# Optimization experiments

Measured on AMD Instinct MI355X. Metric: run time of the kernel, lower is better.

The kernel has to match this reference:

```python
import jax, jax.numpy as jnp
import numpy as np

GRID = 64
N_NODES = GRID * GRID
LN_EPS = 1e-5


def _grid_edge_index(n=GRID):
    ids = np.arange(n * n, dtype=np.int32).reshape(n, n)
    r0, r1 = ids[:, :-1].ravel(), ids[:, 1:].ravel()   # horizontal neighbors
    d0, d1 = ids[:-1, :].ravel(), ids[1:, :].ravel()   # vertical neighbors
    src = np.concatenate([r0, r1, d0, d1])
    dst = np.concatenate([r1, r0, d1, d0])
    return np.stack([src, dst])  # [2, 16128] directed edges


def setup_inputs() -> dict:
    key = jax.random.key(0)
    ks = jax.random.split(key, 6)
    B, C, H, L = 128, 12, 64, 3
    s_in = 1.0 / np.sqrt(C)
    s_h = 1.0 / np.sqrt(H)
    return {
        "x": jax.random.normal(ks[0], (B, C, GRID, GRID), jnp.float32),
        "edge_index": jnp.asarray(_grid_edge_index()),
        "w_in": jax.random.normal(ks[1], (C, H), jnp.float32) * s_in,
        "b_in": jnp.zeros((H,), jnp.float32),
        "w_self": jax.random.normal(ks[2], (L, H, H), jnp.float32) * s_h,
        "w_neigh": jax.random.normal(ks[3], (L, H, H), jnp.float32) * s_h,
        "conv_b": jnp.zeros((L, H), jnp.float32),
        "ln_g": jnp.ones((L, H), jnp.float32),
        "ln_b": jnp.zeros((L, H), jnp.float32),
        "w_head": jax.random.normal(ks[4], (H, 1), jnp.float32) * s_h,
        "b_head": jnp.zeros((1,), jnp.float32),
    }


def reference(x, edge_index, w_in, b_in, w_self, w_neigh, conv_b, ln_g, ln_b, w_head, b_head):
    B = x.shape[0]
    BN = B * N_NODES
    # grid_to_nodes: [B, C, 64, 64] -> [B, N, C]
    nodes = jnp.transpose(x, (0, 2, 3, 1)).reshape(B, N_NODES, -1)
    h = (nodes @ w_in + b_in).reshape(BN, -1)
    # batched_edge_index: replicate with per-graph node offsets
    offs = (jnp.arange(B, dtype=edge_index.dtype) * N_NODES)
    ei = (edge_index[:, None, :] + offs[None, :, None]).reshape(2, -1)
    src, dst = ei[0], ei[1]
    deg = jax.ops.segment_sum(jnp.ones_like(src, dtype=h.dtype), dst, num_segments=BN)
    inv_deg = (1.0 / jnp.maximum(deg, 1.0))[:, None]
    n_layers = w_self.shape[0]
    for l in range(n_layers):
        # SAGE-mean conv: gather src feats, scatter-sum to dst, mean-normalize
        agg = jax.ops.segment_sum(h[src], dst, num_segments=BN) * inv_deg
        hn = h @ w_self[l] + agg @ w_neigh[l] + conv_b[l]
        mu = hn.mean(-1, keepdims=True)
        var = ((hn - mu) ** 2).mean(-1, keepdims=True)
        hn = (hn - mu) * jax.lax.rsqrt(var + LN_EPS) * ln_g[l] + ln_b[l]
        h = h + jax.nn.relu(hn)  # dropout is identity in eval mode
    logit = (h @ w_head + b_head).reshape(B, GRID, GRID)
    return logit
```

## Files before the change

### kernel.cpp

```cpp
#include <hip/hip_runtime.h>

#define GRID_D 64
#define NN (GRID_D * GRID_D)
#define H 64
#define C_IN 12
#define B_SZ 128
#define LN_EPS 1e-5f

typedef _Float16 f16x8 __attribute__((ext_vector_type(8)));
typedef _Float16 f16x4 __attribute__((ext_vector_type(4)));
typedef float    f32x4 __attribute__((ext_vector_type(4)));

#define AS1 __attribute__((address_space(1)))
#define AS3 __attribute__((address_space(3)))

__global__ __launch_bounds__(256) void k_prep(
    const float* __restrict__ ws_, const float* __restrict__ wn_,
    _Float16* __restrict__ wt)
{
    int i = blockIdx.x * 256 + threadIdx.x;
    if (i < 3 * 2 * 4096) {
        int l = i >> 13, g = (i >> 12) & 1, j = (i >> 6) & 63, k = i & 63;
        const float* W = (g ? wn_ : ws_) + l * 4096;
        wt[i] = (_Float16)W[k * 64 + j];
    }
}

__global__ __launch_bounds__(256) void k_inproj(
    const float* __restrict__ x, const float* __restrict__ w_in,
    const float* __restrict__ b_in, _Float16* __restrict__ h)
{
    int bid = blockIdx.x;
    int b = bid >> 6, r = bid & 63;
    __shared__ float xs[C_IN][GRID_D];
    __shared__ float ws[C_IN][H];
    int tid = threadIdx.x;
    const float* xb = x + (size_t)b * C_IN * NN + (size_t)r * GRID_D;
    for (int idx = tid; idx < C_IN * GRID_D; idx += 256) {
        int c = idx >> 6, n = idx & 63;
        xs[c][n] = xb[(size_t)c * NN + n];
        ws[c][n] = w_in[idx];
    }
    __syncthreads();
    int n = tid >> 2;
    int j0 = (tid & 3) * 16;
    float acc[16];
    #pragma unroll
    for (int t = 0; t < 16; ++t) acc[t] = b_in[j0 + t];
    #pragma unroll
    for (int c = 0; c < C_IN; ++c) {
        float xv = xs[c][n];
        #pragma unroll
        for (int t = 0; t < 16; ++t) acc[t] += xv * ws[c][j0 + t];
    }
    _Float16* hp = h + (size_t)(b * NN + r * GRID_D + n) * H + j0;
    f16x8 o0, o1;
    #pragma unroll
    for (int t = 0; t < 8; ++t) { o0[t] = (_Float16)acc[t]; o1[t] = (_Float16)acc[8 + t]; }
    *(f16x8*)hp = o0;
    *(f16x8*)(hp + 8) = o1;
}

__device__ __forceinline__ void stage_row(
    const _Float16* hb, int grow, _Float16* slot, int wv, int ln)
{
    const _Float16* src = hb
        + (((size_t)(grow * GRID_D + wv * 8 + (ln >> 3))) << 6)
        + (((ln & 7) ^ (ln >> 3)) << 3);
    _Float16* dst = slot + wv * 512;
    __builtin_amdgcn_global_load_lds((const AS1 void*)src, (AS3 void*)dst, 16, 0, 0);
}

__global__ __launch_bounds__(768, 3) void k_fused(
    const _Float16* __restrict__ h0, float* __restrict__ logits,
    const _Float16* __restrict__ wtb,
    const float* __restrict__ cb, const float* __restrict__ lg,
    const float* __restrict__ lb,
    const float* __restrict__ w_head, const float* __restrict__ b_head)
{
    __shared__ _Float16 ring[3][4][4096];
    __shared__ float    pl[640];

    int tid = threadIdx.x, ln = tid & 63, wv = tid >> 6;
    int bid = blockIdx.x;
    int img = bid >> 1, chunk = bid & 1;
    int r0 = chunk << 5;
    const _Float16* hb = h0 + ((size_t)img << 18);

    int grp = wv >> 2;
    int ct  = wv & 3;
    int lrow = ln & 15, kgrp = ln >> 4;
    int col = ct * 16 + lrow;
    int cs = col & 7;
    int kq = kgrp * 4;
    bool cl = (col > 0), cr = (col < 63);

    const _Float16* wg = wtb + grp * 8192;
    f16x8 wsf[2][4], wnf[2][4];
    #pragma unroll
    for (int ks = 0; ks < 2; ++ks) {
        int k0 = ks * 32 + kq * 2;
        #pragma unroll
        for (int ft = 0; ft < 4; ++ft) {
            int j = ft * 16 + lrow;
            wsf[ks][ft] = *(const f16x8*)(wg + (j << 6) + k0);
            wnf[ks][ft] = *(const f16x8*)(wg + ((64 + j) << 6) + k0);
        }
    }
    #pragma unroll
    for (int ks = 0; ks < 2; ++ks)
        #pragma unroll
        for (int ft = 0; ft < 4; ++ft)
            asm volatile("" : "+v"(wsf[ks][ft]), "+v"(wnf[ks][ft]));

    if (tid < 576) {
        int l = tid / 192, r = tid % 192;
        pl[tid] = (r < 64) ? cb[l * 64 + r]
                : (r < 128) ? lg[l * 64 + r - 64] : lb[l * 64 + r - 128];
    } else if (tid < 640) {
        pl[tid] = w_head[tid - 576];
    }

    const float* myp = pl + grp * 192;
    float bh = b_head[0];

    int lo0 = (r0 - 3 < 0) ? 0 : r0 - 3, hi0 = (r0 + 34 > 63) ? 63 : r0 + 34;
    int loC, hiC;
    if (grp == 0)      { loC = (r0 - 2 < 0) ? 0 : r0 - 2; hiC = (r0 + 33 > 63) ? 63 : r0 + 33; }
    else if (grp == 1) { loC = (r0 - 1 < 0) ? 0 : r0 - 1; hiC = (r0 + 32 > 63) ? 63 : r0 + 32; }
    else               { loC = r0;                         hiC = r0 + 31; }

    _Float16* rin  = &ring[grp][0][0];
    _Float16* rout = (grp < 2) ? &ring[grp + 1][0][0] : nullptr;

    #pragma unroll 1
    for (int s = 0; s <= 40; ++s) {
        int p0 = r0 - 3 + s;
        if (wv < 8 && p0 >= lo0 && p0 <= hi0)
            stage_row(hb, p0, &ring[0][p0 & 3][0], wv, ln);

        int pr = p0 - 2 * grp - 2;
        if (pr >= loC && pr <= hiC) {
            const _Float16* rc = rin + ((pr & 3) << 12);
            const _Float16* ru = rin + (((pr - 1) & 3) << 12);
            const _Float16* rd = rin + (((pr + 1) & 3) << 12);
            _Float16 hinv = (_Float16)(1.0f / (float)((pr > 0) + (pr < 63) + cl + cr));

            f32x4 acc[4];
            #pragma unroll
            for (int ft = 0; ft < 4; ++ft) acc[ft] = (f32x4){0.f, 0.f, 0.f, 0.f};

            #pragma unroll
            for (int ks = 0; ks < 2; ++ks) {
                int sl = ((ks * 4 + kgrp) ^ cs) << 3;
                f16x8 a = *(const f16x8*)(rc + (col << 6) + sl);
                #pragma unroll
                for (int ft = 0; ft < 4; ++ft)
                    acc[ft] = __builtin_amdgcn_mfma_f32_16x16x32_f16(wsf[ks][ft], a, acc[ft], 0, 0, 0);
            }

            #pragma unroll
            for (int ks = 0; ks < 2; ++ks) {
                int c8 = ks * 4 + kgrp;
                int sl = (c8 ^ cs) << 3;
                f16x8 z = {};
                f16x8 u = (pr > 0)  ? *(const f16x8*)(ru + (col << 6) + sl) : z;
                f16x8 d = (pr < 63) ? *(const f16x8*)(rd + (col << 6) + sl) : z;
                int cm = col - cl;
                f16x8 lv = *(const f16x8*)(rc + (cm << 6) + ((c8 ^ (cm & 7)) << 3));
                if (!cl) lv = z;
                int cp = col + cr;
                f16x8 rv = *(const f16x8*)(rc + (cp << 6) + ((c8 ^ (cp & 7)) << 3));
                if (!cr) rv = z;
                f16x8 sm = (lv + rv) + (u + d);
                f16x8 g;
                #pragma unroll
                for (int e = 0; e < 8; ++e) g[e] = sm[e] * hinv;
                #pragma unroll
                for (int ft = 0; ft < 4; ++ft)
                    acc[ft] = __builtin_amdgcn_mfma_f32_16x16x32_f16(wnf[ks][ft], g, acc[ft], 0, 0, 0);
            }

            float s1 = 0.f, s2 = 0.f;
            #pragma unroll
            for (int ft = 0; ft < 4; ++ft) {
                f32x4 q = *(const f32x4*)&myp[ft * 16 + kq];
                acc[ft] += q;
                #pragma unroll
                for (int t = 0; t < 4; ++t) { float xv = acc[ft][t]; s1 += xv; s2 += xv * xv; }
            }
            s1 += __shfl_xor(s1, 16); s1 += __shfl_xor(s1, 32);
            s2 += __shfl_xor(s2, 16); s2 += __shfl_xor(s2, 32);
            float mu   = s1 * (1.0f / H);
            float var  = s2 * (1.0f / H) - mu * mu;
            float rstd = rsqrtf(var + LN_EPS);

            const _Float16* res = rc + (col << 6);
            if (grp < 2) {
                _Float16* outp = rout + ((pr & 3) << 12) + (col << 6);
                #pragma unroll
                for (int ft = 0; ft < 4; ++ft) {
                    f32x4 lgq = *(const f32x4*)&myp[64 + ft * 16 + kq];
                    f32x4 lbq = *(const f32x4*)&myp[128 + ft * 16 + kq];
                    int slot = (ft * 2 + (kgrp >> 1)) ^ cs;
                    f16x4 rq = *(const f16x4*)(res + (slot << 3) + (kgrp & 1) * 4);
                    f16x4 oq;
                    #pragma unroll
                    for (int t = 0; t < 4; ++t) {
                        float o = (float)rq[t]
                                + fmaxf((acc[ft][t] - mu) * rstd * lgq[t] + lbq[t], 0.f);
                        oq[t] = (_Float16)o;
                    }
                    *(f16x4*)(outp + (slot << 3) + (kgrp & 1) * 4) = oq;
                }
            } else {
                float part = 0.f;
                #pragma unroll
                for (int ft = 0; ft < 4; ++ft) {
                    f32x4 lgq = *(const f32x4*)&myp[64 + ft * 16 + kq];
                    f32x4 lbq = *(const f32x4*)&myp[128 + ft * 16 + kq];
                    f32x4 whq = *(const f32x4*)&pl[576 + ft * 16 + kq];
                    int slot = (ft * 2 + (kgrp >> 1)) ^ cs;
                    f16x4 rq = *(const f16x4*)(res + (slot << 3) + (kgrp & 1) * 4);
                    #pragma unroll
                    for (int t = 0; t < 4; ++t) {
                        float o = (float)rq[t]
                                + fmaxf((acc[ft][t] - mu) * rstd * lgq[t] + lbq[t], 0.f);
                        part += o * whq[t];
                    }
                }
                part += __shfl_xor(part, 16);
                part += __shfl_xor(part, 32);
                if (kgrp == 0)
                    logits[(size_t)img * NN + pr * GRID_D + col] = part + bh;
            }
        }
        __syncthreads();
    }
}

extern "C" void kernel_launch(void* const* d_in, const int* in_sizes, int n_in,
                              void* d_out, int out_size, void* d_ws, size_t ws_size,
                              hipStream_t stream) {
    const float* x      = (const float*)d_in[0];
    const float* w_in   = (const float*)d_in[2];
    const float* b_in   = (const float*)d_in[3];
    const float* w_self = (const float*)d_in[4];
    const float* w_neigh= (const float*)d_in[5];
    const float* conv_b = (const float*)d_in[6];
    const float* ln_g   = (const float*)d_in[7];
    const float* ln_b   = (const float*)d_in[8];
    const float* w_head = (const float*)d_in[9];
    const float* b_head = (const float*)d_in[10];
    float* out = (float*)d_out;

    char* base = (char*)d_ws;
    const size_t HBYTES = (size_t)B_SZ * NN * H * sizeof(_Float16);
    _Float16* h_a = (_Float16*)base;
    _Float16* wtb = (_Float16*)(base + HBYTES);

    k_prep<<<96, 256, 0, stream>>>(w_self, w_neigh, wtb);
    k_inproj<<<B_SZ * GRID_D, 256, 0, stream>>>(x, w_in, b_in, h_a);
    k_fused<<<B_SZ * 2, 768, 0, stream>>>(
        h_a, out, wtb, conv_b, ln_g, ln_b, w_head, b_head);
}
```

Before: 113.5 us.

## Read layer-0 inputs directly from global memory and drop the staging ring

Layer 0 now reads its self and neighbour rows straight from global memory instead of copying them into an LDS ring with async global-to-LDS loads. That removes one of the three ring buffers, so dynamic shared memory drops to two rings plus the parameters, and the launch bound is raised to aim for more resident blocks. The pipeline loop is three steps shorter. In exchange, layer 0 issues redundant global gathers for the neighbour rows (up, down, left, right), which rely on cache hits and add latency exposed inside the wave.

```diff
diff --git a/kernel.cpp b/kernel.cpp
--- a/kernel.cpp
+++ b/kernel.cpp
@@ -11,8 +11,7 @@
 typedef _Float16 f16x4 __attribute__((ext_vector_type(4)));
 typedef float    f32x4 __attribute__((ext_vector_type(4)));
 
-#define AS1 __attribute__((address_space(1)))
-#define AS3 __attribute__((address_space(3)))
+#define SMEM_BYTES (2 * 4 * 4096 * 2 + 640 * 4)
 
 __global__ __launch_bounds__(256) void k_prep(
     const float* __restrict__ ws_, const float* __restrict__ wn_,
@@ -61,31 +60,22 @@
     *(f16x8*)(hp + 8) = o1;
 }
 
-__device__ __forceinline__ void stage_row(
-    const _Float16* hb, int grow, _Float16* slot, int wv, int ln)
-{
-    const _Float16* src = hb
-        + (((size_t)(grow * GRID_D + wv * 8 + (ln >> 3))) << 6)
-        + (((ln & 7) ^ (ln >> 3)) << 3);
-    _Float16* dst = slot + wv * 512;
-    __builtin_amdgcn_global_load_lds((const AS1 void*)src, (AS3 void*)dst, 16, 0, 0);
-}
-
-__global__ __launch_bounds__(768, 3) void k_fused(
+__global__ __launch_bounds__(768, 6) void k_fused(
     const _Float16* __restrict__ h0, float* __restrict__ logits,
     const _Float16* __restrict__ wtb,
     const float* __restrict__ cb, const float* __restrict__ lg,
     const float* __restrict__ lb,
     const float* __restrict__ w_head, const float* __restrict__ b_head)
 {
-    __shared__ _Float16 ring[3][4][4096];
-    __shared__ float    pl[640];
+    extern __shared__ _Float16 smem[];
+    _Float16* ringb = smem;
+    float*    pl    = (float*)(smem + 32768);
 
     int tid = threadIdx.x, ln = tid & 63, wv = tid >> 6;
     int bid = blockIdx.x;
     int img = bid >> 1, chunk = bid & 1;
     int r0 = chunk << 5;
-    const _Float16* hb = h0 + ((size_t)img << 18);
+    const _Float16* hg = h0 + ((size_t)img << 18);
 
     int grp = wv >> 2;
     int ct  = wv & 3;
@@ -120,72 +110,90 @@
     } else if (tid < 640) {
         pl[tid] = w_head[tid - 576];
     }
+    __syncthreads();
 
     const float* myp = pl + grp * 192;
     float bh = b_head[0];
 
-    int lo0 = (r0 - 3 < 0) ? 0 : r0 - 3, hi0 = (r0 + 34 > 63) ? 63 : r0 + 34;
+    int qoff = -2 - 2 * grp;
     int loC, hiC;
     if (grp == 0)      { loC = (r0 - 2 < 0) ? 0 : r0 - 2; hiC = (r0 + 33 > 63) ? 63 : r0 + 33; }
     else if (grp == 1) { loC = (r0 - 1 < 0) ? 0 : r0 - 1; hiC = (r0 + 32 > 63) ? 63 : r0 + 32; }
     else               { loC = r0;                         hiC = r0 + 31; }
 
-    _Float16* rin  = &ring[grp][0][0];
-    _Float16* rout = (grp < 2) ? &ring[grp + 1][0][0] : nullptr;
+    _Float16* rin  = (grp == 1) ? ringb : ringb + 16384;
+    _Float16* rout = (grp == 0) ? ringb : ringb + 16384;
 
     #pragma unroll 1
-    for (int s = 0; s <= 40; ++s) {
-        int p0 = r0 - 3 + s;
-        if (wv < 8 && p0 >= lo0 && p0 <= hi0)
-            stage_row(hb, p0, &ring[0][p0 & 3][0], wv, ln);
-
-        int pr = p0 - 2 * grp - 2;
-        if (pr >= loC && pr <= hiC) {
-            const _Float16* rc = rin + ((pr & 3) << 12);
-            const _Float16* ru = rin + (((pr - 1) & 3) << 12);
-            const _Float16* rd = rin + (((pr + 1) & 3) << 12);
-            _Float16 hinv = (_Float16)(1.0f / (float)((pr > 0) + (pr < 63) + cl + cr));
+    for (int s = 0; s <= 37; ++s) {
+        int q = r0 + qoff + s;
+        if (q >= loC && q <= hiC) {
+            _Float16 hinv = (_Float16)(1.0f / (float)((q > 0) + (q < 63) + cl + cr));
+            f16x8 selfA[2], aggA[2];
+            f16x8 z = {};
+            const _Float16* rp = hg + ((size_t)q << 12);
+            const _Float16* rc = rin + ((q & 3) << 12);
+
+            if (grp == 0) {
+                bool mu = (q > 0), md = (q < 63);
+                #pragma unroll
+                for (int ks = 0; ks < 2; ++ks) {
+                    int k0 = ks * 32 + kq * 2;
+                    const _Float16* pc = rp + (col << 6) + k0;
+                    selfA[ks] = *(const f16x8*)pc;
+                    f16x8 u = mu ? *(const f16x8*)(pc - 4096) : z;
+                    f16x8 d = md ? *(const f16x8*)(pc + 4096) : z;
+                    f16x8 l = cl ? *(const f16x8*)(pc - 64)   : z;
+                    f16x8 r = cr ? *(const f16x8*)(pc + 64)   : z;
+                    f16x8 sm = (l + r) + (u + d);
+                    f16x8 g;
+                    #pragma unroll
+                    for (int e = 0; e < 8; ++e) g[e] = sm[e] * hinv;
+                    aggA[ks] = g;
+                }
+            } else {
+                const _Float16* ru = rin + (((q - 1) & 3) << 12);
+                const _Float16* rd = rin + (((q + 1) & 3) << 12);
+                #pragma unroll
+                for (int ks = 0; ks < 2; ++ks) {
+                    int c8 = ks * 4 + kgrp;
+                    int sl = (c8 ^ cs) << 3;
+                    selfA[ks] = *(const f16x8*)(rc + (col << 6) + sl);
+                    f16x8 u = (q > 0)  ? *(const f16x8*)(ru + (col << 6) + sl) : z;
+                    f16x8 d = (q < 63) ? *(const f16x8*)(rd + (col << 6) + sl) : z;
+                    int cm = col - cl;
+                    f16x8 l = *(const f16x8*)(rc + (cm << 6) + ((c8 ^ (cm & 7)) << 3));
+                    if (!cl) l = z;
+                    int cp = col + cr;
+                    f16x8 r = *(const f16x8*)(rc + (cp << 6) + ((c8 ^ (cp & 7)) << 3));
+                    if (!cr) r = z;
+                    f16x8 sm = (l + r) + (u + d);
+                    f16x8 g;
+                    #pragma unroll
+                    for (int e = 0; e < 8; ++e) g[e] = sm[e] * hinv;
+                    aggA[ks] = g;
+                }
+            }
 
             f32x4 acc[4];
             #pragma unroll
             for (int ft = 0; ft < 4; ++ft) acc[ft] = (f32x4){0.f, 0.f, 0.f, 0.f};
-
-            #pragma unroll
-            for (int ks = 0; ks < 2; ++ks) {
-                int sl = ((ks * 4 + kgrp) ^ cs) << 3;
-                f16x8 a = *(const f16x8*)(rc + (col << 6) + sl);
+            #pragma unroll
+            for (int ks = 0; ks < 2; ++ks)
                 #pragma unroll
                 for (int ft = 0; ft < 4; ++ft)
-                    acc[ft] = __builtin_amdgcn_mfma_f32_16x16x32_f16(wsf[ks][ft], a, acc[ft], 0, 0, 0);
-            }
-
-            #pragma unroll
-            for (int ks = 0; ks < 2; ++ks) {
-                int c8 = ks * 4 + kgrp;
-                int sl = (c8 ^ cs) << 3;
-                f16x8 z = {};
-                f16x8 u = (pr > 0)  ? *(const f16x8*)(ru + (col << 6) + sl) : z;
-                f16x8 d = (pr < 63) ? *(const f16x8*)(rd + (col << 6) + sl) : z;
-                int cm = col - cl;
-                f16x8 lv = *(const f16x8*)(rc + (cm << 6) + ((c8 ^ (cm & 7)) << 3));
-                if (!cl) lv = z;
-                int cp = col + cr;
-                f16x8 rv = *(const f16x8*)(rc + (cp << 6) + ((c8 ^ (cp & 7)) << 3));
-                if (!cr) rv = z;
-                f16x8 sm = (lv + rv) + (u + d);
-                f16x8 g;
-                #pragma unroll
-                for (int e = 0; e < 8; ++e) g[e] = sm[e] * hinv;
+                    acc[ft] = __builtin_amdgcn_mfma_f32_16x16x32_f16(wsf[ks][ft], selfA[ks], acc[ft], 0, 0, 0);
+            #pragma unroll
+            for (int ks = 0; ks < 2; ++ks)
                 #pragma unroll
                 for (int ft = 0; ft < 4; ++ft)
-                    acc[ft] = __builtin_amdgcn_mfma_f32_16x16x32_f16(wnf[ks][ft], g, acc[ft], 0, 0, 0);
-            }
+                    acc[ft] = __builtin_amdgcn_mfma_f32_16x16x32_f16(wnf[ks][ft], aggA[ks], acc[ft], 0, 0, 0);
 
             float s1 = 0.f, s2 = 0.f;
             #pragma unroll
             for (int ft = 0; ft < 4; ++ft) {
-                f32x4 q = *(const f32x4*)&myp[ft * 16 + kq];
-                acc[ft] += q;
+                f32x4 qv = *(const f32x4*)&myp[ft * 16 + kq];
+                acc[ft] += qv;
                 #pragma unroll
                 for (int t = 0; t < 4; ++t) { float xv = acc[ft][t]; s1 += xv; s2 += xv * xv; }
             }
@@ -195,15 +203,18 @@
             float var  = s2 * (1.0f / H) - mu * mu;
             float rstd = rsqrtf(var + LN_EPS);
 
-            const _Float16* res = rc + (col << 6);
             if (grp < 2) {
-                _Float16* outp = rout + ((pr & 3) << 12) + (col << 6);
+                _Float16* outp = rout + ((q & 3) << 12) + (col << 6);
                 #pragma unroll
                 for (int ft = 0; ft < 4; ++ft) {
                     f32x4 lgq = *(const f32x4*)&myp[64 + ft * 16 + kq];
                     f32x4 lbq = *(const f32x4*)&myp[128 + ft * 16 + kq];
                     int slot = (ft * 2 + (kgrp >> 1)) ^ cs;
-                    f16x4 rq = *(const f16x4*)(res + (slot << 3) + (kgrp & 1) * 4);
+                    f16x4 rq;
+                    if (grp == 0)
+                        rq = *(const f16x4*)(rp + (col << 6) + ft * 16 + kq);
+                    else
+                        rq = *(const f16x4*)(rc + (col << 6) + (slot << 3) + (kgrp & 1) * 4);
                     f16x4 oq;
                     #pragma unroll
                     for (int t = 0; t < 4; ++t) {
@@ -221,7 +232,7 @@
                     f32x4 lbq = *(const f32x4*)&myp[128 + ft * 16 + kq];
                     f32x4 whq = *(const f32x4*)&pl[576 + ft * 16 + kq];
                     int slot = (ft * 2 + (kgrp >> 1)) ^ cs;
-                    f16x4 rq = *(const f16x4*)(res + (slot << 3) + (kgrp & 1) * 4);
+                    f16x4 rq = *(const f16x4*)(rc + (col << 6) + (slot << 3) + (kgrp & 1) * 4);
                     #pragma unroll
                     for (int t = 0; t < 4; ++t) {
                         float o = (float)rq[t]
@@ -232,7 +243,7 @@
                 part += __shfl_xor(part, 16);
                 part += __shfl_xor(part, 32);
                 if (kgrp == 0)
-                    logits[(size_t)img * NN + pr * GRID_D + col] = part + bh;
+                    logits[(size_t)img * NN + q * GRID_D + col] = part + bh;
             }
         }
         __syncthreads();
@@ -259,8 +270,11 @@
     _Float16* h_a = (_Float16*)base;
     _Float16* wtb = (_Float16*)(base + HBYTES);
 
+    (void)hipFuncSetAttribute(reinterpret_cast<const void*>(&k_fused),
+                              hipFuncAttributeMaxDynamicSharedMemorySize, SMEM_BYTES);
+
     k_prep<<<96, 256, 0, stream>>>(w_self, w_neigh, wtb);
     k_inproj<<<B_SZ * GRID_D, 256, 0, stream>>>(x, w_in, b_in, h_a);
-    k_fused<<<B_SZ * 2, 768, 0, stream>>>(
+    k_fused<<<B_SZ * 2, 768, SMEM_BYTES, stream>>>(
         h_a, out, wtb, conv_b, ln_g, ln_b, w_head, b_head);
 }
```

Result: slower. 355.6 us (+213.2%).

## Fuse input projection with first SAGE layer and split remaining layers finer

Applied to the files above, without the earlier changes.

Layer 1 of the graph conv moves into the input-projection kernel. Each block recomputes the projection for three neighbouring rows (a one-row halo) in shared memory and runs the layer-1 MFMA, layernorm and residual before writing h1. The fused kernel then handles only layers 2 and 3, splitting each image into four 16-row chunks with 512 threads per block. The aim is to drop the ring stage and pipeline depth in the big kernel and raise parallelism, at the cost of computing the projection three times per row and a shorter pipeline with more halo overhead.

```diff
diff --git a/kernel.cpp b/kernel.cpp
--- a/kernel.cpp
+++ b/kernel.cpp
@@ -26,39 +26,160 @@
     }
 }
 
-__global__ __launch_bounds__(256) void k_inproj(
+__global__ __launch_bounds__(256, 2) void k_inl1(
     const float* __restrict__ x, const float* __restrict__ w_in,
-    const float* __restrict__ b_in, _Float16* __restrict__ h)
+    const float* __restrict__ b_in,
+    const _Float16* __restrict__ wtb,
+    const float* __restrict__ cb, const float* __restrict__ lg,
+    const float* __restrict__ lb,
+    _Float16* __restrict__ h1)
 {
-    int bid = blockIdx.x;
-    int b = bid >> 6, r = bid & 63;
-    __shared__ float xs[C_IN][GRID_D];
-    __shared__ float ws[C_IN][H];
+    __shared__ _Float16 st[3][4096];
+    __shared__ float xs[C_IN][192];
+    __shared__ float ws[C_IN][64];
+    __shared__ float bs[64];
+    __shared__ float pr[192];
+
+    int bid = blockIdx.x, b = bid >> 6, r = bid & 63;
     int tid = threadIdx.x;
-    const float* xb = x + (size_t)b * C_IN * NN + (size_t)r * GRID_D;
-    for (int idx = tid; idx < C_IN * GRID_D; idx += 256) {
-        int c = idx >> 6, n = idx & 63;
-        xs[c][n] = xb[(size_t)c * NN + n];
-        ws[c][n] = w_in[idx];
-    }
+    const float* xb = x + (size_t)b * C_IN * NN;
+
+    for (int idx = tid; idx < C_IN * 192; idx += 256) {
+        int c = idx / 192, q = idx - c * 192;
+        int rr = q >> 6, cc = q & 63;
+        int grow = r - 1 + rr;
+        xs[c][q] = ((unsigned)grow < 64u) ? xb[(size_t)c * NN + grow * 64 + cc] : 0.f;
+    }
+    for (int idx = tid; idx < C_IN * 64; idx += 256) ws[idx >> 6][idx & 63] = w_in[idx];
+    if (tid < 64) bs[tid] = b_in[tid];
+    else if (tid < 256) {
+        int t2 = tid - 64;
+        pr[t2] = (t2 < 64) ? cb[t2] : (t2 < 128) ? lg[t2 - 64] : lb[t2 - 128];
+    }
+
+    int ln = tid & 63, wv = tid >> 6;
+    int lrow = ln & 15, kgrp = ln >> 4, kq = kgrp * 4;
+
+    f16x8 wsf[2][4], wnf[2][4];
+    #pragma unroll
+    for (int ks = 0; ks < 2; ++ks) {
+        int k0 = ks * 32 + kq * 2;
+        #pragma unroll
+        for (int ft = 0; ft < 4; ++ft) {
+            int j = ft * 16 + lrow;
+            wsf[ks][ft] = *(const f16x8*)(wtb + (j << 6) + k0);
+            wnf[ks][ft] = *(const f16x8*)(wtb + ((64 + j) << 6) + k0);
+        }
+    }
+    #pragma unroll
+    for (int ks = 0; ks < 2; ++ks)
+        #pragma unroll
+        for (int ft = 0; ft < 4; ++ft)
+            asm volatile("" : "+v"(wsf[ks][ft]), "+v"(wnf[ks][ft]));
     __syncthreads();
-    int n = tid >> 2;
-    int j0 = (tid & 3) * 16;
-    float acc[16];
-    #pragma unroll
-    for (int t = 0; t < 16; ++t) acc[t] = b_in[j0 + t];
-    #pragma unroll
-    for (int c = 0; c < C_IN; ++c) {
-        float xv = xs[c][n];
-        #pragma unroll
-        for (int t = 0; t < 16; ++t) acc[t] += xv * ws[c][j0 + t];
-    }
-    _Float16* hp = h + (size_t)(b * NN + r * GRID_D + n) * H + j0;
-    f16x8 o0, o1;
-    #pragma unroll
-    for (int t = 0; t < 8; ++t) { o0[t] = (_Float16)acc[t]; o1[t] = (_Float16)acc[8 + t]; }
-    *(f16x8*)hp = o0;
-    *(f16x8*)(hp + 8) = o1;
+
+    {
+        int n = tid >> 2, j0 = (tid & 3) * 16;
+        int sl0 = (((j0 >> 3) ^ (n & 7)) << 3);
+        int sl1 = ((((j0 >> 3) + 1) ^ (n & 7)) << 3);
+        #pragma unroll
+        for (int rr = 0; rr < 3; ++rr) {
+            int grow = r - 1 + rr;
+            float acc[16];
+            #pragma unroll
+            for (int t = 0; t < 16; ++t) acc[t] = bs[j0 + t];
+            #pragma unroll
+            for (int c = 0; c < C_IN; ++c) {
+                float xv = xs[c][rr * 64 + n];
+                #pragma unroll
+                for (int t = 0; t < 16; ++t) acc[t] += xv * ws[c][j0 + t];
+            }
+            bool ok = ((unsigned)grow < 64u);
+            f16x8 lo, hi;
+            #pragma unroll
+            for (int t = 0; t < 8; ++t) {
+                lo[t] = ok ? (_Float16)acc[t]     : (_Float16)0.f;
+                hi[t] = ok ? (_Float16)acc[8 + t] : (_Float16)0.f;
+            }
+            _Float16* dst = &st[rr][n << 6];
+            *(f16x8*)(dst + sl0) = lo;
+            *(f16x8*)(dst + sl1) = hi;
+        }
+    }
+    __syncthreads();
+
+    int col = wv * 16 + lrow;
+    int cs = lrow & 7;
+    bool cl = (col > 0), cr = (col < 63);
+    _Float16 hinv = (_Float16)(1.0f / (float)((r > 0) + (r < 63) + cl + cr));
+    const _Float16* rc = &st[1][0];
+    const _Float16* ru = &st[0][0];
+    const _Float16* rd = &st[2][0];
+
+    f32x4 acc[4];
+    #pragma unroll
+    for (int ft = 0; ft < 4; ++ft) acc[ft] = (f32x4){0.f, 0.f, 0.f, 0.f};
+
+    #pragma unroll
+    for (int ks = 0; ks < 2; ++ks) {
+        int sl = ((ks * 4 + kgrp) ^ cs) << 3;
+        f16x8 a = *(const f16x8*)(rc + (col << 6) + sl);
+        #pragma unroll
+        for (int ft = 0; ft < 4; ++ft)
+            acc[ft] = __builtin_amdgcn_mfma_f32_16x16x32_f16(wsf[ks][ft], a, acc[ft], 0, 0, 0);
+    }
+    #pragma unroll
+    for (int ks = 0; ks < 2; ++ks) {
+        int c8 = ks * 4 + kgrp;
+        int sl = (c8 ^ cs) << 3;
+        f16x8 z = {};
+        f16x8 u = *(const f16x8*)(ru + (col << 6) + sl);
+        f16x8 d = *(const f16x8*)(rd + (col << 6) + sl);
+        int cm = col - cl;
+        f16x8 lv = *(const f16x8*)(rc + (cm << 6) + ((c8 ^ (cm & 7)) << 3));
+        if (!cl) lv = z;
+        int cp = col + cr;
+        f16x8 rv = *(const f16x8*)(rc + (cp << 6) + ((c8 ^ (cp & 7)) << 3));
+        if (!cr) rv = z;
+        f16x8 sm = (lv + rv) + (u + d);
+        f16x8 g;
+        #pragma unroll
+        for (int e = 0; e < 8; ++e) g[e] = sm[e] * hinv;
+        #pragma unroll
+        for (int ft = 0; ft < 4; ++ft)
+            acc[ft] = __builtin_amdgcn_mfma_f32_16x16x32_f16(wnf[ks][ft], g, acc[ft], 0, 0, 0);
+    }
+
+    float s1 = 0.f, s2 = 0.f;
+    #pragma unroll
+    for (int ft = 0; ft < 4; ++ft) {
+        f32x4 qv = *(const f32x4*)&pr[ft * 16 + kq];
+        acc[ft] += qv;
+        #pragma unroll
+        for (int t = 0; t < 4; ++t) { float xv = acc[ft][t]; s1 += xv; s2 += xv * xv; }
+    }
+    s1 += __shfl_xor(s1, 16); s1 += __shfl_xor(s1, 32);
+    s2 += __shfl_xor(s2, 16); s2 += __shfl_xor(s2, 32);
+    float mu   = s1 * (1.0f / H);
+    float var  = s2 * (1.0f / H) - mu * mu;
+    float rstd = rsqrtf(var + LN_EPS);
+
+    _Float16* hp = h1 + (((size_t)(b * NN + r * GRID_D + col)) << 6);
+    #pragma unroll
+    for (int ft = 0; ft < 4; ++ft) {
+        f32x4 lgq = *(const f32x4*)&pr[64 + ft * 16 + kq];
+        f32x4 lbq = *(const f32x4*)&pr[128 + ft * 16 + kq];
+        int slot = (ft * 2 + (kgrp >> 1)) ^ cs;
+        f16x4 rq = *(const f16x4*)(rc + (col << 6) + (slot << 3) + (kgrp & 1) * 4);
+        f16x4 oq;
+        #pragma unroll
+        for (int t = 0; t < 4; ++t) {
+            float o = (float)rq[t]
+                    + fmaxf((acc[ft][t] - mu) * rstd * lgq[t] + lbq[t], 0.f);
+            oq[t] = (_Float16)o;
+        }
+        *(f16x4*)(hp + ft * 16 + kq) = oq;
+    }
 }
 
 __device__ __forceinline__ void stage_row(
@@ -71,31 +192,31 @@
     __builtin_amdgcn_global_load_lds((const AS1 void*)src, (AS3 void*)dst, 16, 0, 0);
 }
 
-__global__ __launch_bounds__(768, 3) void k_fused(
-    const _Float16* __restrict__ h0, float* __restrict__ logits,
+__global__ __launch_bounds__(512, 2) void k_fused2(
+    const _Float16* __restrict__ h1, float* __restrict__ logits,
     const _Float16* __restrict__ wtb,
     const float* __restrict__ cb, const float* __restrict__ lg,
     const float* __restrict__ lb,
     const float* __restrict__ w_head, const float* __restrict__ b_head)
 {
-    __shared__ _Float16 ring[3][4][4096];
-    __shared__ float    pl[640];
+    __shared__ _Float16 ring1[4 * 4096];
+    __shared__ _Float16 ring2[4 * 4096];
+    __shared__ float    pl[448];
 
     int tid = threadIdx.x, ln = tid & 63, wv = tid >> 6;
     int bid = blockIdx.x;
-    int img = bid >> 1, chunk = bid & 1;
-    int r0 = chunk << 5;
-    const _Float16* hb = h0 + ((size_t)img << 18);
+    int img = bid >> 2, chunk = bid & 3;
+    int r0 = chunk << 4;
+    const _Float16* hg = h1 + ((size_t)img << 18);
 
     int grp = wv >> 2;
     int ct  = wv & 3;
-    int lrow = ln & 15, kgrp = ln >> 4;
+    int lrow = ln & 15, kgrp = ln >> 4, kq = kgrp * 4;
     int col = ct * 16 + lrow;
-    int cs = col & 7;
-    int kq = kgrp * 4;
+    int cs = lrow & 7;
     bool cl = (col > 0), cr = (col < 63);
 
-    const _Float16* wg = wtb + grp * 8192;
+    const _Float16* wg = wtb + (grp + 1) * 8192;
     f16x8 wsf[2][4], wnf[2][4];
     #pragma unroll
     for (int ks = 0; ks < 2; ++ks) {
@@ -113,38 +234,37 @@
         for (int ft = 0; ft < 4; ++ft)
             asm volatile("" : "+v"(wsf[ks][ft]), "+v"(wnf[ks][ft]));
 
-    if (tid < 576) {
-        int l = tid / 192, r = tid % 192;
-        pl[tid] = (r < 64) ? cb[l * 64 + r]
-                : (r < 128) ? lg[l * 64 + r - 64] : lb[l * 64 + r - 128];
-    } else if (tid < 640) {
-        pl[tid] = w_head[tid - 576];
-    }
+    if (tid < 384) {
+        int l = tid / 192 + 1, rr = tid % 192;
+        pl[tid] = (rr < 64) ? cb[l * 64 + rr]
+                : (rr < 128) ? lg[l * 64 + rr - 64] : lb[l * 64 + rr - 128];
+    } else if (tid < 448) {
+        pl[tid] = w_head[tid - 384];
+    }
+    __syncthreads();
 
     const float* myp = pl + grp * 192;
     float bh = b_head[0];
 
-    int lo0 = (r0 - 3 < 0) ? 0 : r0 - 3, hi0 = (r0 + 34 > 63) ? 63 : r0 + 34;
-    int loC, hiC;
-    if (grp == 0)      { loC = (r0 - 2 < 0) ? 0 : r0 - 2; hiC = (r0 + 33 > 63) ? 63 : r0 + 33; }
-    else if (grp == 1) { loC = (r0 - 1 < 0) ? 0 : r0 - 1; hiC = (r0 + 32 > 63) ? 63 : r0 + 32; }
-    else               { loC = r0;                         hiC = r0 + 31; }
-
-    _Float16* rin  = &ring[grp][0][0];
-    _Float16* rout = (grp < 2) ? &ring[grp + 1][0][0] : nullptr;
+    int lo0 = (r0 - 2 < 0) ? 0 : r0 - 2;
+    int hi0 = (r0 + 17 > 63) ? 63 : r0 + 17;
+    int loC = grp ? r0 : ((r0 - 1 < 0) ? 0 : r0 - 1);
+    int hiC = grp ? (r0 + 15) : ((r0 + 16 > 63) ? 63 : r0 + 16);
+    const _Float16* rin = grp ? ring2 : ring1;
 
     #pragma unroll 1
-    for (int s = 0; s <= 40; ++s) {
-        int p0 = r0 - 3 + s;
-        if (wv < 8 && p0 >= lo0 && p0 <= hi0)
-            stage_row(hb, p0, &ring[0][p0 & 3][0], wv, ln);
-
-        int pr = p0 - 2 * grp - 2;
-        if (pr >= loC && pr <= hiC) {
-            const _Float16* rc = rin + ((pr & 3) << 12);
-            const _Float16* ru = rin + (((pr - 1) & 3) << 12);
-            const _Float16* rd = rin + (((pr + 1) & 3) << 12);
-            _Float16 hinv = (_Float16)(1.0f / (float)((pr > 0) + (pr < 63) + cl + cr));
+    for (int s = 0; s <= 21; ++s) {
+        int p = r0 - 2 + s;
+        if (p >= lo0 && p <= hi0)
+            stage_row(hg, p, ring1 + ((p & 3) << 12), wv, ln);
+
+        int q = p - 2 - 2 * grp;
+        if (q >= loC && q <= hiC) {
+            _Float16 hinv = (_Float16)(1.0f / (float)((q > 0) + (q < 63) + cl + cr));
+            f16x8 z = {};
+            const _Float16* rc = rin + ((q & 3) << 12);
+            const _Float16* ru = rin + (((q - 1) & 3) << 12);
+            const _Float16* rd = rin + (((q + 1) & 3) << 12);
 
             f32x4 acc[4];
             #pragma unroll
@@ -158,14 +278,12 @@
                 for (int ft = 0; ft < 4; ++ft)
                     acc[ft] = __builtin_amdgcn_mfma_f32_16x16x32_f16(wsf[ks][ft], a, acc[ft], 0, 0, 0);
             }
-
             #pragma unroll
             for (int ks = 0; ks < 2; ++ks) {
                 int c8 = ks * 4 + kgrp;
                 int sl = (c8 ^ cs) << 3;
-                f16x8 z = {};
-                f16x8 u = (pr > 0)  ? *(const f16x8*)(ru + (col << 6) + sl) : z;
-                f16x8 d = (pr < 63) ? *(const f16x8*)(rd + (col << 6) + sl) : z;
+                f16x8 u = (q > 0)  ? *(const f16x8*)(ru + (col << 6) + sl) : z;
+                f16x8 d = (q < 63) ? *(const f16x8*)(rd + (col << 6) + sl) : z;
                 int cm = col - cl;
                 f16x8 lv = *(const f16x8*)(rc + (cm << 6) + ((c8 ^ (cm & 7)) << 3));
                 if (!cl) lv = z;
@@ -184,8 +302,8 @@
             float s1 = 0.f, s2 = 0.f;
             #pragma unroll
             for (int ft = 0; ft < 4; ++ft) {
-                f32x4 q = *(const f32x4*)&myp[ft * 16 + kq];
-                acc[ft] += q;
+                f32x4 qv = *(const f32x4*)&myp[ft * 16 + kq];
+                acc[ft] += qv;
                 #pragma unroll
                 for (int t = 0; t < 4; ++t) { float xv = acc[ft][t]; s1 += xv; s2 += xv * xv; }
             }
@@ -195,15 +313,14 @@
             float var  = s2 * (1.0f / H) - mu * mu;
             float rstd = rsqrtf(var + LN_EPS);
 
-            const _Float16* res = rc + (col << 6);
-            if (grp < 2) {
-                _Float16* outp = rout + ((pr & 3) << 12) + (col << 6);
+            if (grp == 0) {
+                _Float16* outp = ring2 + ((q & 3) << 12) + (col << 6);
                 #pragma unroll
                 for (int ft = 0; ft < 4; ++ft) {
                     f32x4 lgq = *(const f32x4*)&myp[64 + ft * 16 + kq];
                     f32x4 lbq = *(const f32x4*)&myp[128 + ft * 16 + kq];
                     int slot = (ft * 2 + (kgrp >> 1)) ^ cs;
-                    f16x4 rq = *(const f16x4*)(res + (slot << 3) + (kgrp & 1) * 4);
+                    f16x4 rq = *(const f16x4*)(rc + (col << 6) + (slot << 3) + (kgrp & 1) * 4);
                     f16x4 oq;
                     #pragma unroll
                     for (int t = 0; t < 4; ++t) {
@@ -219,9 +336,9 @@
                 for (int ft = 0; ft < 4; ++ft) {
                     f32x4 lgq = *(const f32x4*)&myp[64 + ft * 16 + kq];
                     f32x4 lbq = *(const f32x4*)&myp[128 + ft * 16 + kq];
-                    f32x4 whq = *(const f32x4*)&pl[576 + ft * 16 + kq];
+                    f32x4 whq = *(const f32x4*)&pl[384 + ft * 16 + kq];
                     int slot = (ft * 2 + (kgrp >> 1)) ^ cs;
-                    f16x4 rq = *(const f16x4*)(res + (slot << 3) + (kgrp & 1) * 4);
+                    f16x4 rq = *(const f16x4*)(rc + (col << 6) + (slot << 3) + (kgrp & 1) * 4);
                     #pragma unroll
                     for (int t = 0; t < 4; ++t) {
                         float o = (float)rq[t]
@@ -232,7 +349,7 @@
                 part += __shfl_xor(part, 16);
                 part += __shfl_xor(part, 32);
                 if (kgrp == 0)
-                    logits[(size_t)img * NN + pr * GRID_D + col] = part + bh;
+                    logits[(size_t)img * NN + q * GRID_D + col] = part + bh;
             }
         }
         __syncthreads();
@@ -256,11 +373,12 @@
 
     char* base = (char*)d_ws;
     const size_t HBYTES = (size_t)B_SZ * NN * H * sizeof(_Float16);
-    _Float16* h_a = (_Float16*)base;
+    _Float16* h1  = (_Float16*)base;
     _Float16* wtb = (_Float16*)(base + HBYTES);
 
     k_prep<<<96, 256, 0, stream>>>(w_self, w_neigh, wtb);
-    k_inproj<<<B_SZ * GRID_D, 256, 0, stream>>>(x, w_in, b_in, h_a);
-    k_fused<<<B_SZ * 2, 768, 0, stream>>>(
-        h_a, out, wtb, conv_b, ln_g, ln_b, w_head, b_head);
-}
+    k_inl1<<<B_SZ * GRID_D, 256, 0, stream>>>(
+        x, w_in, b_in, wtb, conv_b, ln_g, ln_b, h1);
+    k_fused2<<<B_SZ * 4, 512, 0, stream>>>(
+        h1, out, wtb, conv_b, ln_g, ln_b, w_head, b_head);
+}
```

Result: slower. 284.5 us (+150.6%).

## Add dedicated stager waves to fused kernel and raise MFMA priority

Applied to the files above, without the earlier changes.

Grows the fused block from 768 to 1024 threads, with four extra waves that only issue global-to-LDS row loads, each loading two column chunks. The twelve compute waves no longer issue staging loads themselves, and they raise their scheduling priority around the MFMA section with s_setprio. A barrier is added after the parameter load into shared memory. The aim is to take load issue off the compute waves' critical path, at the cost of more threads per block, possible register or occupancy limits under launch_bounds(1024,3), and idle stager waves at every barrier.

```diff
diff --git a/kernel.cpp b/kernel.cpp
--- a/kernel.cpp
+++ b/kernel.cpp
@@ -61,17 +61,7 @@
     *(f16x8*)(hp + 8) = o1;
 }
 
-__device__ __forceinline__ void stage_row(
-    const _Float16* hb, int grow, _Float16* slot, int wv, int ln)
-{
-    const _Float16* src = hb
-        + (((size_t)(grow * GRID_D + wv * 8 + (ln >> 3))) << 6)
-        + (((ln & 7) ^ (ln >> 3)) << 3);
-    _Float16* dst = slot + wv * 512;
-    __builtin_amdgcn_global_load_lds((const AS1 void*)src, (AS3 void*)dst, 16, 0, 0);
-}
-
-__global__ __launch_bounds__(768, 3) void k_fused(
+__global__ __launch_bounds__(1024, 3) void k_fused(
     const _Float16* __restrict__ h0, float* __restrict__ logits,
     const _Float16* __restrict__ wtb,
     const float* __restrict__ cb, const float* __restrict__ lg,
@@ -85,33 +75,35 @@
     int bid = blockIdx.x;
     int img = bid >> 1, chunk = bid & 1;
     int r0 = chunk << 5;
-    const _Float16* hb = h0 + ((size_t)img << 18);
-
-    int grp = wv >> 2;
+    const _Float16* hg = h0 + ((size_t)img << 18);
+
+    bool stager = (wv < 4);
+    int grp = stager ? 0 : (wv >> 2) - 1;
     int ct  = wv & 3;
-    int lrow = ln & 15, kgrp = ln >> 4;
+    int lrow = ln & 15, kgrp = ln >> 4, kq = kgrp * 4;
     int col = ct * 16 + lrow;
-    int cs = col & 7;
-    int kq = kgrp * 4;
+    int cs = lrow & 7;
     bool cl = (col > 0), cr = (col < 63);
 
-    const _Float16* wg = wtb + grp * 8192;
     f16x8 wsf[2][4], wnf[2][4];
-    #pragma unroll
-    for (int ks = 0; ks < 2; ++ks) {
-        int k0 = ks * 32 + kq * 2;
+    if (!stager) {
+        const _Float16* wg = wtb + grp * 8192;
         #pragma unroll
-        for (int ft = 0; ft < 4; ++ft) {
-            int j = ft * 16 + lrow;
-            wsf[ks][ft] = *(const f16x8*)(wg + (j << 6) + k0);
-            wnf[ks][ft] = *(const f16x8*)(wg + ((64 + j) << 6) + k0);
+        for (int ks = 0; ks < 2; ++ks) {
+            int k0 = ks * 32 + kq * 2;
+            #pragma unroll
+            for (int ft = 0; ft < 4; ++ft) {
+                int j = ft * 16 + lrow;
+                wsf[ks][ft] = *(const f16x8*)(wg + (j << 6) + k0);
+                wnf[ks][ft] = *(const f16x8*)(wg + ((64 + j) << 6) + k0);
+            }
         }
-    }
-    #pragma unroll
-    for (int ks = 0; ks < 2; ++ks)
         #pragma unroll
-        for (int ft = 0; ft < 4; ++ft)
-            asm volatile("" : "+v"(wsf[ks][ft]), "+v"(wnf[ks][ft]));
+        for (int ks = 0; ks < 2; ++ks)
+            #pragma unroll
+            for (int ft = 0; ft < 4; ++ft)
+                asm volatile("" : "+v"(wsf[ks][ft]), "+v"(wnf[ks][ft]));
+    }
 
     if (tid < 576) {
         int l = tid / 192, r = tid % 192;
@@ -120,119 +112,135 @@
     } else if (tid < 640) {
         pl[tid] = w_head[tid - 576];
     }
+    __syncthreads();
 
     const float* myp = pl + grp * 192;
     float bh = b_head[0];
 
-    int lo0 = (r0 - 3 < 0) ? 0 : r0 - 3, hi0 = (r0 + 34 > 63) ? 63 : r0 + 34;
+    int lo0 = (r0 - 3 < 0) ? 0 : r0 - 3;
+    int hi0 = (r0 + 34 > 63) ? 63 : r0 + 34;
     int loC, hiC;
     if (grp == 0)      { loC = (r0 - 2 < 0) ? 0 : r0 - 2; hiC = (r0 + 33 > 63) ? 63 : r0 + 33; }
     else if (grp == 1) { loC = (r0 - 1 < 0) ? 0 : r0 - 1; hiC = (r0 + 32 > 63) ? 63 : r0 + 32; }
     else               { loC = r0;                         hiC = r0 + 31; }
 
-    _Float16* rin  = &ring[grp][0][0];
-    _Float16* rout = (grp < 2) ? &ring[grp + 1][0][0] : nullptr;
+    const _Float16* rin = &ring[grp][0][0];
+    _Float16* rout      = (grp < 2) ? &ring[grp + 1][0][0] : nullptr;
+
+    int snode = ln >> 3;
+    int sslot = ((ln & 7) ^ snode) << 3;
 
     #pragma unroll 1
     for (int s = 0; s <= 40; ++s) {
-        int p0 = r0 - 3 + s;
-        if (wv < 8 && p0 >= lo0 && p0 <= hi0)
-            stage_row(hb, p0, &ring[0][p0 & 3][0], wv, ln);
-
-        int pr = p0 - 2 * grp - 2;
-        if (pr >= loC && pr <= hiC) {
-            const _Float16* rc = rin + ((pr & 3) << 12);
-            const _Float16* ru = rin + (((pr - 1) & 3) << 12);
-            const _Float16* rd = rin + (((pr + 1) & 3) << 12);
-            _Float16 hinv = (_Float16)(1.0f / (float)((pr > 0) + (pr < 63) + cl + cr));
-
-            f32x4 acc[4];
-            #pragma unroll
-            for (int ft = 0; ft < 4; ++ft) acc[ft] = (f32x4){0.f, 0.f, 0.f, 0.f};
-
-            #pragma unroll
-            for (int ks = 0; ks < 2; ++ks) {
-                int sl = ((ks * 4 + kgrp) ^ cs) << 3;
-                f16x8 a = *(const f16x8*)(rc + (col << 6) + sl);
-                #pragma unroll
-                for (int ft = 0; ft < 4; ++ft)
-                    acc[ft] = __builtin_amdgcn_mfma_f32_16x16x32_f16(wsf[ks][ft], a, acc[ft], 0, 0, 0);
+        int p = r0 - 3 + s;
+        if (stager) {
+            if (p >= lo0 && p <= hi0) {
+                _Float16* slot = &ring[0][p & 3][0];
+                #pragma unroll
+                for (int i = 0; i < 2; ++i) {
+                    int c = wv * 2 + i;
+                    const _Float16* src = hg
+                        + (((size_t)(p * GRID_D + c * 8 + snode)) << 6) + sslot;
+                    __builtin_amdgcn_global_load_lds(
+                        (const AS1 void*)src, (AS3 void*)(slot + c * 512), 16, 0, 0);
+                }
             }
-
-            #pragma unroll
-            for (int ks = 0; ks < 2; ++ks) {
-                int c8 = ks * 4 + kgrp;
-                int sl = (c8 ^ cs) << 3;
+        } else {
+            int q = p - 2 - 2 * grp;
+            if (q >= loC && q <= hiC) {
+                _Float16 hinv = (_Float16)(1.0f / (float)((q > 0) + (q < 63) + cl + cr));
                 f16x8 z = {};
-                f16x8 u = (pr > 0)  ? *(const f16x8*)(ru + (col << 6) + sl) : z;
-                f16x8 d = (pr < 63) ? *(const f16x8*)(rd + (col << 6) + sl) : z;
-                int cm = col - cl;
-                f16x8 lv = *(const f16x8*)(rc + (cm << 6) + ((c8 ^ (cm & 7)) << 3));
-                if (!cl) lv = z;
-                int cp = col + cr;
-                f16x8 rv = *(const f16x8*)(rc + (cp << 6) + ((c8 ^ (cp & 7)) << 3));
-                if (!cr) rv = z;
-                f16x8 sm = (lv + rv) + (u + d);
-                f16x8 g;
-                #pragma unroll
-                for (int e = 0; e < 8; ++e) g[e] = sm[e] * hinv;
-                #pragma unroll
-                for (int ft = 0; ft < 4; ++ft)
-                    acc[ft] = __builtin_amdgcn_mfma_f32_16x16x32_f16(wnf[ks][ft], g, acc[ft], 0, 0, 0);
-            }
-
-            float s1 = 0.f, s2 = 0.f;
-            #pragma unroll
-            for (int ft = 0; ft < 4; ++ft) {
-                f32x4 q = *(const f32x4*)&myp[ft * 16 + kq];
-                acc[ft] += q;
-                #pragma unroll
-                for (int t = 0; t < 4; ++t) { float xv = acc[ft][t]; s1 += xv; s2 += xv * xv; }
-            }
-            s1 += __shfl_xor(s1, 16); s1 += __shfl_xor(s1, 32);
-            s2 += __shfl_xor(s2, 16); s2 += __shfl_xor(s2, 32);
-            float mu   = s1 * (1.0f / H);
-            float var  = s2 * (1.0f / H) - mu * mu;
-            float rstd = rsqrtf(var + LN_EPS);
-
-            const _Float16* res = rc + (col << 6);
-            if (grp < 2) {
-                _Float16* outp = rout + ((pr & 3) << 12) + (col << 6);
+                const _Float16* rc = rin + ((q & 3) << 12);
+                const _Float16* ru = rin + (((q - 1) & 3) << 12);
+                const _Float16* rd = rin + (((q + 1) & 3) << 12);
+
+                f32x4 acc[4];
+                #pragma unroll
+                for (int ft = 0; ft < 4; ++ft) acc[ft] = (f32x4){0.f, 0.f, 0.f, 0.f};
+
+                __builtin_amdgcn_s_setprio(1);
+                #pragma unroll
+                for (int ks = 0; ks < 2; ++ks) {
+                    int sl = ((ks * 4 + kgrp) ^ cs) << 3;
+                    f16x8 a = *(const f16x8*)(rc + (col << 6) + sl);
+                    #pragma unroll
+                    for (int ft = 0; ft < 4; ++ft)
+                        acc[ft] = __builtin_amdgcn_mfma_f32_16x16x32_f16(wsf[ks][ft], a, acc[ft], 0, 0, 0);
+                }
+                #pragma unroll
+                for (int ks = 0; ks < 2; ++ks) {
+                    int c8 = ks * 4 + kgrp;
+                    int sl = (c8 ^ cs) << 3;
+                    f16x8 u = (q > 0)  ? *(const f16x8*)(ru + (col << 6) + sl) : z;
+                    f16x8 d = (q < 63) ? *(const f16x8*)(rd + (col << 6) + sl) : z;
+                    int cm = col - cl;
+                    f16x8 lv = *(const f16x8*)(rc + (cm << 6) + ((c8 ^ (cm & 7)) << 3));
+                    if (!cl) lv = z;
+                    int cp = col + cr;
+                    f16x8 rv = *(const f16x8*)(rc + (cp << 6) + ((c8 ^ (cp & 7)) << 3));
+                    if (!cr) rv = z;
+                    f16x8 sm = (lv + rv) + (u + d);
+                    f16x8 g;
+                    #pragma unroll
+                    for (int e = 0; e < 8; ++e) g[e] = sm[e] * hinv;
+                    #pragma unroll
+                    for (int ft = 0; ft < 4; ++ft)
+                        acc[ft] = __builtin_amdgcn_mfma_f32_16x16x32_f16(wnf[ks][ft], g, acc[ft], 0, 0, 0);
+                }
+                __builtin_amdgcn_s_setprio(0);
+
+                float s1 = 0.f, s2 = 0.f;
                 #pragma unroll
                 for (int ft = 0; ft < 4; ++ft) {
-                    f32x4 lgq = *(const f32x4*)&myp[64 + ft * 16 + kq];
-                    f32x4 lbq = *(const f32x4*)&myp[128 + ft * 16 + kq];
-                    int slot = (ft * 2 + (kgrp >> 1)) ^ cs;
-                    f16x4 rq = *(const f16x4*)(res + (slot << 3) + (kgrp & 1) * 4);
-                    f16x4 oq;
-                    #pragma unroll
-                    for (int t = 0; t < 4; ++t) {
-                        float o = (float)rq[t]
-                                + fmaxf((acc[ft][t] - mu) * rstd * lgq[t] + lbq[t], 0.f);
-                        oq[t] = (_Float16)o;
+                    f32x4 qv = *(const f32x4*)&myp[ft * 16 + kq];
+                    acc[ft] += qv;
+                    #pragma unroll
+                    for (int t = 0; t < 4; ++t) { float xv = acc[ft][t]; s1 += xv; s2 += xv * xv; }
+                }
+                s1 += __shfl_xor(s1, 16); s1 += __shfl_xor(s1, 32);
+                s2 += __shfl_xor(s2, 16); s2 += __shfl_xor(s2, 32);
+                float mu   = s1 * (1.0f / H);
+                float var  = s2 * (1.0f / H) - mu * mu;
+                float rstd = rsqrtf(var + LN_EPS);
+
+                if (grp < 2) {
+                    _Float16* outp = rout + ((q & 3) << 12) + (col << 6);
+                    #pragma unroll
+                    for (int ft = 0; ft < 4; ++ft) {
+                        f32x4 lgq = *(const f32x4*)&myp[64 + ft * 16 + kq];
+                        f32x4 lbq = *(const f32x4*)&myp[128 + ft * 16 + kq];
+                        int slot = (ft * 2 + (kgrp >> 1)) ^ cs;
+                        f16x4 rq = *(const f16x4*)(rc + (col << 6) + (slot << 3) + (kgrp & 1) * 4);
+                        f16x4 oq;
+                        #pragma unroll
+                        for (int t = 0; t < 4; ++t) {
+                            float o = (float)rq[t]
+                                    + fmaxf((acc[ft][t] - mu) * rstd * lgq[t] + lbq[t], 0.f);
+                            oq[t] = (_Float16)o;
+                        }
+                        *(f16x4*)(outp + (slot << 3) + (kgrp & 1) * 4) = oq;
                     }
-                    *(f16x4*)(outp + (slot << 3) + (kgrp & 1) * 4) = oq;
-                }
-            } else {
-                float part = 0.f;
-                #pragma unroll
-                for (int ft = 0; ft < 4; ++ft) {
-                    f32x4 lgq = *(const f32x4*)&myp[64 + ft * 16 + kq];
-                    f32x4 lbq = *(const f32x4*)&myp[128 + ft * 16 + kq];
-                    f32x4 whq = *(const f32x4*)&pl[576 + ft * 16 + kq];
-                    int slot = (ft * 2 + (kgrp >> 1)) ^ cs;
-                    f16x4 rq = *(const f16x4*)(res + (slot << 3) + (kgrp & 1) * 4);
-                    #pragma unroll
-                    for (int t = 0; t < 4; ++t) {
-                        float o = (float)rq[t]
-                                + fmaxf((acc[ft][t] - mu) * rstd * lgq[t] + lbq[t], 0.f);
-                        part += o * whq[t];
+                } else {
+                    float part = 0.f;
+                    #pragma unroll
+                    for (int ft = 0; ft < 4; ++ft) {
+                        f32x4 lgq = *(const f32x4*)&myp[64 + ft * 16 + kq];
+                        f32x4 lbq = *(const f32x4*)&myp[128 + ft * 16 + kq];
+                        f32x4 whq = *(const f32x4*)&pl[576 + ft * 16 + kq];
+                        int slot = (ft * 2 + (kgrp >> 1)) ^ cs;
+                        f16x4 rq = *(const f16x4*)(rc + (col << 6) + (slot << 3) + (kgrp & 1) * 4);
+                        #pragma unroll
+                        for (int t = 0; t < 4; ++t) {
+                            float o = (float)rq[t]
+                                    + fmaxf((acc[ft][t] - mu) * rstd * lgq[t] + lbq[t], 0.f);
+                            part += o * whq[t];
+                        }
                     }
-                }
-                part += __shfl_xor(part, 16);
-                part += __shfl_xor(part, 32);
-                if (kgrp == 0)
-                    logits[(size_t)img * NN + pr * GRID_D + col] = part + bh;
+                    part += __shfl_xor(part, 16);
+                    part += __shfl_xor(part, 32);
+                    if (kgrp == 0)
+                        logits[(size_t)img * NN + q * GRID_D + col] = part + bh;
+                }
             }
         }
         __syncthreads();
@@ -261,6 +269,6 @@
 
     k_prep<<<96, 256, 0, stream>>>(w_self, w_neigh, wtb);
     k_inproj<<<B_SZ * GRID_D, 256, 0, stream>>>(x, w_in, b_in, h_a);
-    k_fused<<<B_SZ * 2, 768, 0, stream>>>(
+    k_fused<<<B_SZ * 2, 1024, 0, stream>>>(
         h_a, out, wtb, conv_b, ln_g, ln_b, w_head, b_head);
 }
```

Measured after the change: 146.4 us. 28.9% more time.
